# Optimization experiments

Hardware: AMD Instinct MI355X
Metric: run time of the kernel (lower is better)

The kernel has to match this reference:

```python
import jax, jax.numpy as jnp
import numpy as np
import math

N, C, W, H = 8, 1024, 1024, 16
D = C // H  # head size = 64


def setup_inputs() -> dict:
    key = jax.random.key(0)
    ks = jax.random.split(key, 7)
    s = 1.0 / math.sqrt(C)
    return {
        "hidden_states": jax.random.normal(ks[0], (N, C, W), jnp.float32),
        "attention_mask": jnp.zeros((N, 1, 1, W), jnp.float32),
        "wq": jax.random.normal(ks[1], (C, C), jnp.float32) * s,
        "bq": jax.random.normal(ks[2], (C,), jnp.float32) * 0.02,
        "wk": jax.random.normal(ks[3], (C, C), jnp.float32) * s,
        "bk": jax.random.normal(ks[4], (C,), jnp.float32) * 0.02,
        "wv": jax.random.normal(ks[5], (C, C), jnp.float32) * s,
        "bv": jax.random.normal(ks[6], (C,), jnp.float32) * 0.02,
    }


def reference(hidden_states, attention_mask, wq, bq, wk, bk, wv, bv):
    # conv1d(kernel=1, groups=1) == per-position GEMM: [N,C,W] x [Cout,Cin] -> [N,Cout,W]
    q = jnp.einsum('ncw,oc->now', hidden_states, wq) + bq[None, :, None]
    k = jnp.einsum('ncw,oc->now', hidden_states, wk) + bk[None, :, None]
    v = jnp.einsum('ncw,oc->now', hidden_states, wv) + bv[None, :, None]
    # split heads: [N,C,W] -> [N,H,D,W]
    q = q.reshape(N, H, D, W).transpose(0, 1, 3, 2)  # [N,H,W,D]
    k = k.reshape(N, H, D, W)                         # [N,H,D,W]
    v = v.reshape(N, H, D, W).transpose(0, 1, 3, 2)  # [N,H,W,D]
    scores = jnp.einsum('nhqd,nhdk->nhqk', q, k) / math.sqrt(D)
    scores = scores + attention_mask  # broadcast [N,1,1,W]
    probs = jax.nn.softmax(scores, axis=-1)
    ctx = jnp.einsum('nhqk,nhkd->nhqd', probs, v)    # [N,H,W,D]
    # merge heads back to [N,C,W]
    return ctx.transpose(0, 1, 3, 2).reshape(N, C, W)
```

## Files before the change

### kernel.cpp

```cpp
#include <hip/hip_runtime.h>
#include <hip/hip_bf16.h>

typedef __bf16 bf16x8 __attribute__((ext_vector_type(8)));
typedef __bf16 bf16x4 __attribute__((ext_vector_type(4)));
typedef float f32x4 __attribute__((ext_vector_type(4)));

#define N_ 8
#define C_ 1024
#define W_ 1024
#define H_ 16
#define D_ 64

typedef __attribute__((address_space(3))) void lds_void;
typedef const __attribute__((address_space(1))) void gbl_void;
static __device__ __forceinline__ void gload_lds16(const void* g, void* l) {
    __builtin_amdgcn_global_load_lds((gbl_void*)g, (lds_void*)l, 16, 0, 0);
}

__global__ __launch_bounds__(256)
void prep(const float* __restrict__ hs,
          const float* __restrict__ wq, const float* __restrict__ wk,
          const float* __restrict__ wv,
          __bf16* __restrict__ Xt, __bf16* __restrict__ Wb) {
    __shared__ float tile[64][68];
    const int b = blockIdx.x;
    const int t = threadIdx.x;
    if (b < 2048) {
        const int bx = b & 15, by = (b >> 4) & 15, bz = b >> 8;
        const long bin  = (long)bz * C_ * W_;
        const long bout = (long)bz * W_ * C_;
        const int w0 = bx * 64, c0 = by * 64;
        const int rr = t >> 4;
        const int cg = (t & 15) * 4;
        #pragma unroll
        for (int it = 0; it < 4; ++it) {
            const int cr = it * 16 + rr;
            f32x4 v = *(const f32x4*)(const void*)(hs + bin + (long)(c0 + cr) * W_ + w0 + cg);
            *(f32x4*)&tile[cr][cg] = v;
        }
        __syncthreads();
        #pragma unroll
        for (int it = 0; it < 4; ++it) {
            const int wr = it * 16 + rr;
            bf16x4 o;
            #pragma unroll
            for (int u = 0; u < 4; ++u) o[u] = (__bf16)tile[cg + u][wr];
            *(bf16x4*)(void*)(Xt + bout + (long)(w0 + wr) * C_ + c0 + cg) = o;
        }
    } else {
        const int cb = b - 2048;
        const int wsel = cb >> 9;
        const int x = cb & 511;
        const float* s = wsel == 0 ? wq : (wsel == 1 ? wk : wv);
        __bf16* d = Wb + (long)wsel * C_ * C_;
        const long i = ((long)x * 256 + t) * 8;
        f32x4 a = *(const f32x4*)(const void*)(s + i);
        f32x4 bb = *(const f32x4*)(const void*)(s + i + 4);
        bf16x8 v;
        #pragma unroll
        for (int u = 0; u < 4; ++u) { v[u] = (__bf16)a[u]; v[u + 4] = (__bf16)bb[u]; }
        *(bf16x8*)(void*)(d + i) = v;
    }
}

template<int OUT_T>
static __device__ __forceinline__
void gemm_body(const __bf16* __restrict__ Aw, const __bf16* __restrict__ Xn,
               const float* __restrict__ bias, __bf16* __restrict__ Pn,
               const int o0, const int w0,
               __bf16* __restrict__ As, __bf16* __restrict__ Bs) {
    const int tid = threadIdx.x;
    const int wv = tid >> 6, lane = tid & 63;
    const int l15 = lane & 15, quad = lane >> 4;
    const int wr = (wv >> 1) * 64, wc = (wv & 1) * 64;
    const int lr4 = lane >> 2;
    const int lc4 = lane & 3;

    f32x4 acc[4][4] = {};

    auto stage = [&](int k0, int b) {
        #pragma unroll
        for (int j = 0; j < 2; ++j) {
            const int seg = wv * 2 + j;
            const int r = seg * 16 + lr4;
            const int q = lc4 ^ (r & 3);
            gload_lds16(Aw + (long)(o0 + r) * C_ + k0 + q * 8, As + b * 4096 + seg * 512);
            gload_lds16(Xn + (long)(w0 + r) * C_ + k0 + q * 8, Bs + b * 4096 + seg * 512);
        }
    };

    stage(0, 0);
    asm volatile("s_waitcnt vmcnt(0)" ::: "memory");
    __syncthreads();

    for (int ti = 0; ti < 32; ++ti) {
        const int cur = ti & 1;
        if (ti + 1 < 32) stage((ti + 1) * 32, cur ^ 1);

        const __bf16* Ab = As + cur * 4096;
        const __bf16* Bb = Bs + cur * 4096;
        bf16x8 af[4], bf[4];
        #pragma unroll
        for (int mt = 0; mt < 4; ++mt) {
            const int R = wr + mt * 16 + l15;
            const int pos = quad ^ (R & 3);
            af[mt] = *(const bf16x8*)(const void*)&Ab[R * 32 + pos * 8];
        }
        #pragma unroll
        for (int nt = 0; nt < 4; ++nt) {
            const int R = wc + nt * 16 + l15;
            const int pos = quad ^ (R & 3);
            bf[nt] = *(const bf16x8*)(const void*)&Bb[R * 32 + pos * 8];
        }
        #pragma unroll
        for (int mt = 0; mt < 4; ++mt)
            #pragma unroll
            for (int nt = 0; nt < 4; ++nt) {
                if (OUT_T == 0)
                    acc[mt][nt] = __builtin_amdgcn_mfma_f32_16x16x32_bf16(af[mt], bf[nt], acc[mt][nt], 0, 0, 0);
                else
                    acc[mt][nt] = __builtin_amdgcn_mfma_f32_16x16x32_bf16(bf[nt], af[mt], acc[mt][nt], 0, 0, 0);
            }
        asm volatile("s_waitcnt vmcnt(0)" ::: "memory");
        __syncthreads();
    }

    #pragma unroll
    for (int mt = 0; mt < 4; ++mt) {
        #pragma unroll
        for (int nt = 0; nt < 4; ++nt) {
            #pragma unroll
            for (int rg = 0; rg < 4; ++rg) {
                if (OUT_T == 0) {
                    const int col = w0 + wc + nt * 16 + l15;
                    const int row = o0 + wr + mt * 16 + quad * 4 + rg;
                    Pn[(long)row * W_ + col] = (__bf16)(acc[mt][nt][rg] + bias[row]);
                } else {
                    const int o = o0 + wr + mt * 16 + l15;
                    const int w = w0 + wc + nt * 16 + quad * 4 + rg;
                    Pn[(long)w * C_ + o] = (__bf16)(acc[mt][nt][rg] + bias[o]);
                }
            }
        }
    }
}

__global__ __launch_bounds__(256)
void gemm_qkv(const __bf16* __restrict__ Wb, const __bf16* __restrict__ Xt,
              const float* __restrict__ bq, const float* __restrict__ bk,
              const float* __restrict__ bv,
              __bf16* __restrict__ Qt, __bf16* __restrict__ Kt,
              __bf16* __restrict__ Vb) {
    __shared__ __align__(16) __bf16 As[2 * 4096];
    __shared__ __align__(16) __bf16 Bs[2 * 4096];
    const int f = blockIdx.x;
    const int n = f & 7;
    const int j = f >> 3;
    const int which = j >> 6;
    const int t = j & 63;
    const int o0 = (t >> 3) * 128;
    const int w0 = (t & 7) * 128;
    const size_t SZ = (size_t)C_ * W_;
    const size_t WSZ = (size_t)C_ * C_;
    const __bf16* Xn = Xt + (size_t)n * SZ;
    const __bf16* Aw = Wb + (size_t)which * WSZ;
    if (which < 2)
        gemm_body<1>(Aw, Xn, which ? bk : bq, (which ? Kt : Qt) + n * SZ, o0, w0, As, Bs);
    else
        gemm_body<0>(Aw, Xn, bv, Vb + n * SZ, o0, w0, As, Bs);
}

__global__ __launch_bounds__(256)
void flash_attn(const __bf16* __restrict__ Qt,
                const __bf16* __restrict__ Kt,
                const __bf16* __restrict__ V,
                const float* __restrict__ mask,
                float* __restrict__ out) {
    __shared__ __align__(16) __bf16 Pl[4 * 16 * 64];
    __shared__ __align__(16) __bf16 Ks[2][64 * 64];
    __shared__ __align__(16) __bf16 Vs[2][64 * 64];

    const int f = blockIdx.x;
    const int g = (f & 7) + ((f >> 6) << 3);
    const int m = (f >> 3) & 7;
    const int n = g >> 4, h = g & 15;
    const int q0 = m * 128;

    const int tid = threadIdx.x;
    const int wave = tid >> 6, lane = tid & 63;
    const int l15 = lane & 15, quad = lane >> 4;
    const int lr8 = lane >> 3, lp = lane & 7;
    const long nqk = (long)n * W_ * C_;
    const long nv = (long)n * C_ * W_;
    const int hD = h * D_;
    const float* mrow = mask + (long)n * W_;
    constexpr float SC = 0.125f * 1.44269504f;
    constexpr float L2E = 1.44269504f;

    char* plb = (char*)Pl + wave * 2048;
    const int swz = (l15 & 7) << 4;
    const int plrow = l15 * 128;

    bf16x8 aq[2][2];
    #pragma unroll
    for (int qs = 0; qs < 2; ++qs)
        #pragma unroll
        for (int dc = 0; dc < 2; ++dc)
            aq[qs][dc] = *(const bf16x8*)(const void*)
                (Qt + nqk + (long)(q0 + wave * 32 + qs * 16 + l15) * C_ + hD + dc * 32 + quad * 8);

    f32x4 o_acc[2][4] = {};
    float l_ln[2] = {};

    auto stage = [&](int kt, int b) {
        #pragma unroll
        for (int jj = 0; jj < 2; ++jj) {
            const int seg = wave * 2 + jj;
            const int r = seg * 8 + lr8;
            const int q = lp ^ (r & 7);
            gload_lds16(Kt + nqk + (long)(kt + r) * C_ + hD + q * 8, &Ks[b][seg * 512]);
            gload_lds16(V + nv + (long)(hD + r) * W_ + kt + q * 8, &Vs[b][seg * 512]);
        }
    };

    stage(0, 0);

    for (int ti = 0; ti < W_ / 64; ++ti) {
        const int kt = ti * 64;
        const int cur = ti & 1;
        asm volatile("s_waitcnt vmcnt(0)" ::: "memory");
        __syncthreads();
        if (ti + 1 < W_ / 64) stage(kt + 64, cur ^ 1);

        bf16x8 bk[4][2];
        #pragma unroll
        for (int ks = 0; ks < 4; ++ks)
            #pragma unroll
            for (int dc = 0; dc < 2; ++dc) {
                const int R = ks * 16 + l15;
                const int pos = (dc * 4 + quad) ^ (R & 7);
                bk[ks][dc] = *(const bf16x8*)(const void*)&Ks[cur][R * 64 + pos * 8];
            }
        f32x4 mk2[4];
        #pragma unroll
        for (int ks = 0; ks < 4; ++ks) {
            f32x4 mv = *(const f32x4*)(const void*)(mrow + kt + ks * 16 + quad * 4);
            #pragma unroll
            for (int rg = 0; rg < 4; ++rg) mk2[ks][rg] = mv[rg] * L2E;
        }

        f32x4 s2[2][4] = {};
        #pragma unroll
        for (int qs = 0; qs < 2; ++qs)
            #pragma unroll
            for (int ks = 0; ks < 4; ++ks)
                #pragma unroll
                for (int dc = 0; dc < 2; ++dc)
                    s2[qs][ks] = __builtin_amdgcn_mfma_f32_16x16x32_bf16(bk[ks][dc], aq[qs][dc], s2[qs][ks], 0, 0, 0);

        #pragma unroll
        for (int qs = 0; qs < 2; ++qs)
            #pragma unroll
            for (int ks = 0; ks < 4; ++ks) {
                #pragma unroll
                for (int rg = 0; rg < 4; ++rg)
                    s2[qs][ks][rg] = __builtin_amdgcn_exp2f(s2[qs][ks][rg] * SC + mk2[ks][rg]);
                l_ln[qs] += (s2[qs][ks][0] + s2[qs][ks][1]) + (s2[qs][ks][2] + s2[qs][ks][3]);
            }

        bf16x8 ap[2][2];
        #pragma unroll
        for (int qs = 0; qs < 2; ++qs) {
            #pragma unroll
            for (int ks = 0; ks < 4; ++ks) {
                bf16x4 p4;
                #pragma unroll
                for (int rg = 0; rg < 4; ++rg) p4[rg] = (__bf16)s2[qs][ks][rg];
                *(bf16x4*)(void*)(plb + plrow + ((ks * 32 + quad * 8) ^ swz)) = p4;
            }
            #pragma unroll
            for (int kc = 0; kc < 2; ++kc)
                ap[qs][kc] = *(const bf16x8*)(const void*)
                    (plb + plrow + ((kc * 64 + quad * 16) ^ swz));
        }

        bf16x8 bv[4][2];
        #pragma unroll
        for (int ds = 0; ds < 4; ++ds)
            #pragma unroll
            for (int kc = 0; kc < 2; ++kc) {
                const int R = ds * 16 + l15;
                const int pos = (kc * 4 + quad) ^ (R & 7);
                bv[ds][kc] = *(const bf16x8*)(const void*)&Vs[cur][R * 64 + pos * 8];
            }
        #pragma unroll
        for (int qs = 0; qs < 2; ++qs)
            #pragma unroll
            for (int ds = 0; ds < 4; ++ds)
                #pragma unroll
                for (int kc = 0; kc < 2; ++kc)
                    o_acc[qs][ds] = __builtin_amdgcn_mfma_f32_16x16x32_bf16(ap[qs][kc], bv[ds][kc], o_acc[qs][ds], 0, 0, 0);
    }

    #pragma unroll
    for (int qs = 0; qs < 2; ++qs) {
        float l = l_ln[qs];
        l += __shfl_xor(l, 16, 64);
        l += __shfl_xor(l, 32, 64);
        const float linv = 1.0f / l;
        #pragma unroll
        for (int rg = 0; rg < 4; ++rg) {
            const float inv = __shfl(linv, quad * 4 + rg, 64);
            #pragma unroll
            for (int ds = 0; ds < 4; ++ds)
                out[nv + (long)(hD + ds * 16 + l15) * W_ + q0 + wave * 32 + qs * 16 + quad * 4 + rg]
                    = o_acc[qs][ds][rg] * inv;
        }
    }
}

extern "C" void kernel_launch(void* const* d_in, const int* in_sizes, int n_in,
                              void* d_out, int out_size, void* d_ws, size_t ws_size,
                              hipStream_t stream) {
    (void)in_sizes; (void)n_in; (void)out_size; (void)ws_size;
    const float* hs   = (const float*)d_in[0];
    const float* mask = (const float*)d_in[1];
    const float* wq   = (const float*)d_in[2];
    const float* bq   = (const float*)d_in[3];
    const float* wk   = (const float*)d_in[4];
    const float* bk   = (const float*)d_in[5];
    const float* wv   = (const float*)d_in[6];
    const float* bv   = (const float*)d_in[7];
    float* out = (float*)d_out;

    const size_t SZ = (size_t)N_ * C_ * W_;
    const size_t WSZ = (size_t)C_ * C_;
    __bf16* Wb = (__bf16*)d_ws;
    __bf16* Xt = Wb + 3 * WSZ;
    __bf16* Qt = Xt + SZ;
    __bf16* Kt = Qt + SZ;
    __bf16* Vb = Kt + SZ;

    prep<<<dim3(2048 + 1536), 256, 0, stream>>>(hs, wq, wk, wv, Xt, Wb);

    gemm_qkv<<<dim3(1536), 256, 0, stream>>>(Wb, Xt, bq, bk, bv, Qt, Kt, Vb);

    flash_attn<<<dim3(1024), 256, 0, stream>>>(Qt, Kt, Vb, mask, out);
}
```

Before: 235.5 us.

## Split attention K/V staging with partial waits and retune GEMM LDS swizzle

The attention loop now stages K and V tiles separately. Each uses its own `s_waitcnt vmcnt(2)` plus barrier, so the next K tile loads while the current V tile is still in flight, and V is prefetched after the softmax phase. This aims to overlap global-to-LDS traffic with QK and PV compute instead of draining all loads at the top of every iteration. The QKV GEMM XOR swizzle changes from `R&3` to `(R>>1)&3` to reduce LDS bank conflicts on 16-byte fragment reads. Both main loops get `#pragma unroll 1`. Risks are the extra barrier per iteration and manual vmcnt accounting that interacts with the other global loads in the loop.

```diff
diff --git a/kernel.cpp b/kernel.cpp
--- a/kernel.cpp
+++ b/kernel.cpp
@@ -83,7 +83,7 @@
         for (int j = 0; j < 2; ++j) {
             const int seg = wv * 2 + j;
             const int r = seg * 16 + lr4;
-            const int q = lc4 ^ (r & 3);
+            const int q = lc4 ^ ((lr4 >> 1) & 3);
             gload_lds16(Aw + (long)(o0 + r) * C_ + k0 + q * 8, As + b * 4096 + seg * 512);
             gload_lds16(Xn + (long)(w0 + r) * C_ + k0 + q * 8, Bs + b * 4096 + seg * 512);
         }
@@ -93,6 +93,7 @@
     asm volatile("s_waitcnt vmcnt(0)" ::: "memory");
     __syncthreads();
 
+    #pragma unroll 1
     for (int ti = 0; ti < 32; ++ti) {
         const int cur = ti & 1;
         if (ti + 1 < 32) stage((ti + 1) * 32, cur ^ 1);
@@ -103,13 +104,13 @@
         #pragma unroll
         for (int mt = 0; mt < 4; ++mt) {
             const int R = wr + mt * 16 + l15;
-            const int pos = quad ^ (R & 3);
+            const int pos = quad ^ ((R >> 1) & 3);
             af[mt] = *(const bf16x8*)(const void*)&Ab[R * 32 + pos * 8];
         }
         #pragma unroll
         for (int nt = 0; nt < 4; ++nt) {
             const int R = wc + nt * 16 + l15;
-            const int pos = quad ^ (R & 3);
+            const int pos = quad ^ ((R >> 1) & 3);
             bf[nt] = *(const bf16x8*)(const void*)&Bb[R * 32 + pos * 8];
         }
         #pragma unroll
@@ -212,25 +213,37 @@
     f32x4 o_acc[2][4] = {};
     float l_ln[2] = {};
 
-    auto stage = [&](int kt, int b) {
+    auto stageK = [&](int kt, int b) {
         #pragma unroll
         for (int jj = 0; jj < 2; ++jj) {
             const int seg = wave * 2 + jj;
             const int r = seg * 8 + lr8;
             const int q = lp ^ (r & 7);
             gload_lds16(Kt + nqk + (long)(kt + r) * C_ + hD + q * 8, &Ks[b][seg * 512]);
+        }
+    };
+    auto stageV = [&](int kt, int b) {
+        #pragma unroll
+        for (int jj = 0; jj < 2; ++jj) {
+            const int seg = wave * 2 + jj;
+            const int r = seg * 8 + lr8;
+            const int q = lp ^ (r & 7);
             gload_lds16(V + nv + (long)(hD + r) * W_ + kt + q * 8, &Vs[b][seg * 512]);
         }
     };
 
-    stage(0, 0);
-
+    stageK(0, 0);
+    stageV(0, 0);
+
+    #pragma unroll 1
     for (int ti = 0; ti < W_ / 64; ++ti) {
         const int kt = ti * 64;
         const int cur = ti & 1;
-        asm volatile("s_waitcnt vmcnt(0)" ::: "memory");
-        __syncthreads();
-        if (ti + 1 < W_ / 64) stage(kt + 64, cur ^ 1);
+
+        asm volatile("s_waitcnt vmcnt(2)" ::: "memory");
+        __builtin_amdgcn_s_barrier();
+        asm volatile("" ::: "memory");
+        if (ti + 1 < W_ / 64) stageK(kt + 64, cur ^ 1);
 
         bf16x8 bk[4][2];
         #pragma unroll
@@ -283,6 +296,12 @@
                 ap[qs][kc] = *(const bf16x8*)(const void*)
                     (plb + plrow + ((kc * 64 + quad * 16) ^ swz));
         }
+
+        if (ti + 1 < W_ / 64) asm volatile("s_waitcnt vmcnt(2)" ::: "memory");
+        else                  asm volatile("s_waitcnt vmcnt(0)" ::: "memory");
+        __builtin_amdgcn_s_barrier();
+        asm volatile("" ::: "memory");
+        if (ti + 1 < W_ / 64) stageV(kt + 64, cur ^ 1);
 
         bf16x8 bv[4][2];
         #pragma unroll
```

Result: no change. 235.1 us (-0.2%).
